# Optimization experiments

Hardware: AMD Instinct MI355X
Metric: run time of the kernel (lower is better)

The kernel has to match this reference:

```python
import jax, jax.numpy as jnp
import numpy as np

FEATS = 1024
HEAD = 16
MLP_HIDDEN = 4096
HEAD_DIM = FEATS // HEAD
SQRT_D = float(FEATS) ** 0.5  # module scales by sqrt(feats), not sqrt(head_dim)
LN_EPS = 1e-5


def layer_norm(x, g, b):
    mu = jnp.mean(x, axis=-1, keepdims=True)
    var = jnp.mean(jnp.square(x - mu), axis=-1, keepdims=True)
    return (x - mu) * jax.lax.rsqrt(var + LN_EPS) * g + b


def setup_inputs() -> dict:
    key = jax.random.key(0)
    ks = jax.random.split(key, 12)
    s = 1.0 / np.sqrt(FEATS)
    s2 = 1.0 / np.sqrt(MLP_HIDDEN)
    return {
        "x": jax.random.normal(ks[0], (2, 2048, FEATS), dtype=jnp.float32),
        "ln1_g": jnp.ones((FEATS,), jnp.float32),
        "ln1_b": jnp.zeros((FEATS,), jnp.float32),
        "wq": jax.random.normal(ks[1], (FEATS, FEATS), jnp.float32) * s,
        "bq": jnp.zeros((FEATS,), jnp.float32),
        "wk": jax.random.normal(ks[2], (FEATS, FEATS), jnp.float32) * s,
        "bk": jnp.zeros((FEATS,), jnp.float32),
        "wv": jax.random.normal(ks[3], (FEATS, FEATS), jnp.float32) * s,
        "bv": jnp.zeros((FEATS,), jnp.float32),
        "wo": jax.random.normal(ks[4], (FEATS, FEATS), jnp.float32) * s,
        "bo": jnp.zeros((FEATS,), jnp.float32),
        "ln2_g": jnp.ones((FEATS,), jnp.float32),
        "ln2_b": jnp.zeros((FEATS,), jnp.float32),
        "w1": jax.random.normal(ks[5], (MLP_HIDDEN, FEATS), jnp.float32) * s,
        "b1": jnp.zeros((MLP_HIDDEN,), jnp.float32),
        "w2": jax.random.normal(ks[6], (FEATS, MLP_HIDDEN), jnp.float32) * s2,
        "b2": jnp.zeros((FEATS,), jnp.float32),
    }


def reference(x, ln1_g, ln1_b, wq, bq, wk, bk, wv, bv, wo, bo,
              ln2_g, ln2_b, w1, b1, w2, b2):
    b, n, f = x.shape
    h = layer_norm(x, ln1_g, ln1_b)
    # qkv projections (torch Linear: y = x @ W.T + b)
    q = (h @ wq.T + bq).reshape(b, n, HEAD, HEAD_DIM).transpose(0, 2, 1, 3)
    k = (h @ wk.T + bk).reshape(b, n, HEAD, HEAD_DIM).transpose(0, 2, 1, 3)
    v = (h @ wv.T + bv).reshape(b, n, HEAD, HEAD_DIM).transpose(0, 2, 1, 3)
    score = jax.nn.softmax(jnp.einsum('bhif,bhjf->bhij', q, k) / SQRT_D, axis=-1)
    attn = jnp.einsum('bhij,bhjf->bihf', score, v).reshape(b, n, f)
    o = attn @ wo.T + bo
    out1 = o + x
    h2 = layer_norm(out1, ln2_g, ln2_b)
    mlp = jax.nn.relu(jax.nn.relu(h2 @ w1.T + b1) @ w2.T + b2)
    return mlp + out1
```

## Files before the change

### kernel.cpp

```cpp
#include <hip/hip_runtime.h>
#include <hip/hip_bf16.h>

#define FEATS 1024
#define NH 16
#define HD 64
#define SEQ 2048
#define BATCH 2
#define MTOT (BATCH*SEQ)
#define MLPH 4096
#define QSCALE 0.04508422277369218f

typedef __attribute__((ext_vector_type(8))) short bf16x8;
typedef __attribute__((ext_vector_type(4))) float f32x4;

static_assert(sizeof(bf16x8) == 16, "bf16x8 must be 16B");

__device__ __forceinline__ unsigned short f2bf(float f) {
    unsigned int u = __float_as_uint(f);
    unsigned int lsb = (u >> 16) & 1u;
    u += 0x7fffu + lsb;
    return (unsigned short)(u >> 16);
}
__device__ __forceinline__ float bf2f(unsigned short u) {
    return __uint_as_float((unsigned)u << 16);
}

#define ASYNC16(GP, LP) __builtin_amdgcn_global_load_lds( \
    (const __attribute__((address_space(1))) void*)(GP),  \
    (__attribute__((address_space(3))) void*)(LP), 16, 0, 0)

#define WAIT_VM(N) asm volatile("s_waitcnt vmcnt(" #N ")" ::: "memory")

__global__ __launch_bounds__(256) void cvt_all_kernel(
    const float* __restrict__ wq, const float* __restrict__ wk,
    const float* __restrict__ wv, const float* __restrict__ wo,
    const float* __restrict__ w1, const float* __restrict__ w2,
    unsigned short* __restrict__ dst) {
    const size_t i = ((size_t)blockIdx.x * 256 + threadIdx.x) * 4;
    const size_t MB = (size_t)1024 * 1024;
    const float* s;
    size_t off;
    float sc = 1.0f;
    if (i < MB)            { s = wq; off = i;          sc = QSCALE; }
    else if (i < 2 * MB)   { s = wk; off = i - MB; }
    else if (i < 3 * MB)   { s = wv; off = i - 2 * MB; }
    else if (i < 4 * MB)   { s = wo; off = i - 3 * MB; }
    else if (i < 8 * MB)   { s = w1; off = i - 4 * MB; }
    else                   { s = w2; off = i - 8 * MB; }
    float4 v = *(const float4*)(s + off);
    ushort4 o;
    o.x = f2bf(v.x * sc); o.y = f2bf(v.y * sc);
    o.z = f2bf(v.z * sc); o.w = f2bf(v.w * sc);
    *(ushort4*)(dst + i) = o;
}

__global__ __launch_bounds__(256) void concat3_kernel(const float* __restrict__ a,
                                                      const float* __restrict__ b,
                                                      const float* __restrict__ c,
                                                      float* __restrict__ o) {
    int i = blockIdx.x * 256 + threadIdx.x;
    float v = (i < 1024) ? a[i] * QSCALE : ((i < 2048) ? b[i - 1024] : c[i - 2048]);
    o[i] = v;
}

template <bool INBF16>
__global__ __launch_bounds__(256) void ln_kernel(const void* __restrict__ xin,
                                                 const float* __restrict__ g,
                                                 const float* __restrict__ bta,
                                                 unsigned short* __restrict__ h) {
    __shared__ float red[8];
    const int row = blockIdx.x;
    const int t = threadIdx.x;
    float4 v;
    if (INBF16) {
        const unsigned short* xr = (const unsigned short*)xin + (size_t)row * FEATS;
        ushort4 u = ((const ushort4*)xr)[t];
        v.x = bf2f(u.x); v.y = bf2f(u.y); v.z = bf2f(u.z); v.w = bf2f(u.w);
    } else {
        const float* xr = (const float*)xin + (size_t)row * FEATS;
        v = ((const float4*)xr)[t];
    }
    float s  = v.x + v.y + v.z + v.w;
    float ss = v.x * v.x + v.y * v.y + v.z * v.z + v.w * v.w;
#pragma unroll
    for (int off = 1; off < 64; off <<= 1) {
        s  += __shfl_xor(s, off);
        ss += __shfl_xor(ss, off);
    }
    const int w = t >> 6;
    if ((t & 63) == 0) { red[w] = s; red[4 + w] = ss; }
    __syncthreads();
    s  = red[0] + red[1] + red[2] + red[3];
    ss = red[4] + red[5] + red[6] + red[7];
    const float mu  = s * (1.f / FEATS);
    const float var = ss * (1.f / FEATS) - mu * mu;
    const float rs  = rsqrtf(var + 1e-5f);
    float4 gv = ((const float4*)g)[t];
    float4 bv = ((const float4*)bta)[t];
    ushort4 ov;
    ov.x = f2bf((v.x - mu) * rs * gv.x + bv.x);
    ov.y = f2bf((v.y - mu) * rs * gv.y + bv.y);
    ov.z = f2bf((v.z - mu) * rs * gv.z + bv.z);
    ov.w = f2bf((v.w - mu) * rs * gv.w + bv.w);
    ((ushort4*)h)[(size_t)row * (FEATS / 4) + t] = ov;
}

template <int DEPTH, bool RELU, bool ADDF32, bool ADDBF16, bool OUTBF16, bool VTRANS>
__global__ __launch_bounds__(256, (DEPTH == 2 ? 4 : DEPTH == 3 ? 3 : 2))
void gemm_kernel(const unsigned short* __restrict__ A,
                 const unsigned short* __restrict__ W,
                 const float* __restrict__ bias,
                 const void* __restrict__ addend,
                 void* __restrict__ outp,
                 unsigned short* __restrict__ vtp,
                 int M, int N, int K, int gx) {
    __shared__ unsigned short lds[DEPTH][2][128 * 32];

    const int t = threadIdx.x;
    const int w = t >> 6, lane = t & 63;
    const int wr = w >> 1, wc = w & 1;
    const int li = lane & 15, lj = lane >> 4;

    const int nwg = gridDim.x;
    const int cpx = nwg >> 3;
    const int wg = blockIdx.x;
    const int swz = (wg & 7) * cpx + (wg >> 3);
    const int mb = (swz / gx) * 128, nb = (swz % gx) * 128;

    const int srow = lane >> 2;
    const int scg = ((lane & 3) ^ (srow & 3)) * 8;
    const unsigned short* gA = A + (size_t)(mb + w * 16 + srow) * K + scg;
    const unsigned short* gB = W + (size_t)(nb + w * 16 + srow) * K + scg;
    const size_t half = (size_t)64 * K;
    const int lbase = w * 512 + lane * 8;

    const int rsw = (lj ^ (li & 3)) * 8;

    const int nt = K >> 5;

#define STAGE(BUF, K0)                                             \
    do {                                                           \
        unsigned short* la_ = &lds[BUF][0][lbase];                 \
        unsigned short* lb_ = &lds[BUF][1][lbase];                 \
        ASYNC16(gA + (K0), la_);                                   \
        ASYNC16(gA + half + (K0), la_ + 2048);                     \
        ASYNC16(gB + (K0), lb_);                                   \
        ASYNC16(gB + half + (K0), lb_ + 2048);                     \
    } while (0)

#pragma unroll
    for (int j = 0; j < DEPTH - 1; ++j)
        STAGE(j, j * 32);
    if constexpr (DEPTH == 2)      WAIT_VM(0);
    else if constexpr (DEPTH == 3) WAIT_VM(4);
    else                           WAIT_VM(8);
    __builtin_amdgcn_s_barrier();

    f32x4 acc[4][4] = {};

    for (int i = 0; i < nt; ++i) {
        const int cur = i % DEPTH;
        const unsigned short* Al = &lds[cur][0][0];
        const unsigned short* Bl = &lds[cur][1][0];

        bf16x8 af[4], bfr[4];
#pragma unroll
        for (int m = 0; m < 4; m++)
            af[m] = *(const bf16x8*)(Al + (wr * 64 + m * 16 + li) * 32 + rsw);
#pragma unroll
        for (int n = 0; n < 4; n++)
            bfr[n] = *(const bf16x8*)(Bl + (wc * 64 + n * 16 + li) * 32 + rsw);

        const int pft = i + DEPTH - 1;
        if (pft < nt) STAGE(pft % DEPTH, pft * 32);

#pragma unroll
        for (int m = 0; m < 4; m++)
#pragma unroll
            for (int n = 0; n < 4; n++)
                acc[m][n] = __builtin_amdgcn_mfma_f32_16x16x32_bf16(af[m], bfr[n], acc[m][n], 0, 0, 0);

        if (i + 1 < nt) {
            const int avail = (nt - 2) - i;
            const int rem = avail < (DEPTH - 2) ? avail : (DEPTH - 2);
            if (rem >= DEPTH - 2) {
                if constexpr (DEPTH == 2)      WAIT_VM(0);
                else if constexpr (DEPTH == 3) WAIT_VM(4);
                else                           WAIT_VM(8);
            }
            else if (rem == 1) WAIT_VM(4);
            else               WAIT_VM(0);
            __builtin_amdgcn_s_barrier();
        }
    }
#undef STAGE

#pragma unroll
    for (int m = 0; m < 4; m++) {
#pragma unroll
        for (int n = 0; n < 4; n++) {
            const int col = nb + wc * 64 + n * 16 + li;
            const float bv = bias[col];
            if (VTRANS && col >= 2048) {
                const int d2 = col - 2048;
                const int h2 = d2 >> 6, dd = d2 & 63;
                const int rowb = mb + wr * 64 + m * 16 + lj * 4;
                const int bb = rowb >> 11;
                const int s0 = rowb & (SEQ - 1);
                const int pos = (s0 & ~31) | (((s0 >> 2) & 3) << 3) | (((s0 >> 4) & 1) << 2);
                ushort4 vv;
                vv.x = f2bf(acc[m][n][0] + bv);
                vv.y = f2bf(acc[m][n][1] + bv);
                vv.z = f2bf(acc[m][n][2] + bv);
                vv.w = f2bf(acc[m][n][3] + bv);
                *(ushort4*)(vtp + ((size_t)(bb * NH + h2) * HD + dd) * SEQ + pos) = vv;
                continue;
            }
#pragma unroll
            for (int r = 0; r < 4; r++) {
                const int row = mb + wr * 64 + m * 16 + lj * 4 + r;
                float v = acc[m][n][r] + bv;
                if (RELU) v = fmaxf(v, 0.f);
                if (ADDF32)
                    v += ((const float*)addend)[(size_t)row * N + col];
                if (ADDBF16)
                    v += bf2f(((const unsigned short*)addend)[(size_t)row * N + col]);
                if (OUTBF16)
                    ((unsigned short*)outp)[(size_t)row * N + col] = f2bf(v);
                else
                    ((float*)outp)[(size_t)row * N + col] = v;
            }
        }
    }
}

__global__ __launch_bounds__(256, 4)
void attn_kernel(const unsigned short* __restrict__ qkv,
                 const unsigned short* __restrict__ vt,
                 unsigned short* __restrict__ out) {
    constexpr int LK = 72;
    __shared__ unsigned short Kl[2][64 * LK];
    __shared__ unsigned short Vtl[2][64 * LK];

    const int bh = blockIdx.x;
    const int b = bh >> 4, h = bh & 15;
    const int q0 = blockIdx.y * 128;
    const int t = threadIdx.x, w = t >> 6, lane = t & 63;
    const int li = lane & 15, lj = lane >> 4;

    const size_t rstr = 3 * FEATS;
    const unsigned short* qkvb = qkv + (size_t)(b * SEQ) * rstr;
    const unsigned short* ksrc = qkvb + FEATS + h * HD;
    const unsigned short* vsrc = vt + (size_t)bh * HD * SEQ;

    bf16x8 aq[2][2];
#pragma unroll
    for (int hh = 0; hh < 2; hh++)
#pragma unroll
        for (int kk = 0; kk < 2; kk++)
            aq[hh][kk] = *(const bf16x8*)(qkvb +
                (size_t)(q0 + w * 32 + hh * 16 + li) * rstr + h * HD + kk * 32 + lj * 8);

    f32x4 o[2][4] = {};
    f32x4 oS[2] = {};

    const short onebf = (short)0x3F80;
    const bf16x8 ones = {onebf, onebf, onebf, onebf, onebf, onebf, onebf, onebf};

    const int sr = t >> 2, sc = (t & 3) * 16;
    const unsigned short* kg = ksrc + (size_t)sr * rstr + sc;
    const unsigned short* vg = vsrc + (size_t)sr * SEQ + sc;
    const int ldo = sr * LK + sc;

    const int nt = SEQ / 64;

    {
        bf16x8 k0 = *(const bf16x8*)kg;
        bf16x8 k1 = *(const bf16x8*)(kg + 8);
        bf16x8 v0 = *(const bf16x8*)vg;
        bf16x8 v1 = *(const bf16x8*)(vg + 8);
        *(bf16x8*)(&Kl[0][ldo])      = k0;
        *(bf16x8*)(&Kl[0][ldo + 8])  = k1;
        *(bf16x8*)(&Vtl[0][ldo])     = v0;
        *(bf16x8*)(&Vtl[0][ldo + 8]) = v1;
    }

    int cur = 0;
    for (int i = 0; i < nt; ++i) {
        bf16x8 kr0, kr1, vr0, vr1;
        if (i + 1 < nt) {
            const unsigned short* kn = kg + (size_t)(i + 1) * 64 * rstr;
            const unsigned short* vn = vg + (i + 1) * 64;
            kr0 = *(const bf16x8*)kn;
            kr1 = *(const bf16x8*)(kn + 8);
            vr0 = *(const bf16x8*)vn;
            vr1 = *(const bf16x8*)(vn + 8);
        }

        asm volatile("s_waitcnt lgkmcnt(0)" ::: "memory");
        __builtin_amdgcn_s_barrier();

        const unsigned short* Kc = Kl[cur];
        const unsigned short* Vc = Vtl[cur];

        f32x4 s[2][4];
        __builtin_amdgcn_s_setprio(1);
#pragma unroll
        for (int n = 0; n < 4; n++) {
            bf16x8 k0 = *(const bf16x8*)(Kc + (n * 16 + li) * LK + lj * 8);
            bf16x8 k1 = *(const bf16x8*)(Kc + (n * 16 + li) * LK + 32 + lj * 8);
#pragma unroll
            for (int hh = 0; hh < 2; hh++) {
                f32x4 acc = {};
                acc = __builtin_amdgcn_mfma_f32_16x16x32_bf16(k0, aq[hh][0], acc, 0, 0, 0);
                acc = __builtin_amdgcn_mfma_f32_16x16x32_bf16(k1, aq[hh][1], acc, 0, 0, 0);
                s[hh][n] = acc;
            }
        }
        __builtin_amdgcn_s_setprio(0);

        bf16x8 A[2][2];
#pragma unroll
        for (int hh = 0; hh < 2; hh++)
#pragma unroll
            for (int kk = 0; kk < 2; kk++) {
                float p[8];
#pragma unroll
                for (int r = 0; r < 4; r++) {
                    p[r]     = exp2f(s[hh][2 * kk][r]);
                    p[4 + r] = exp2f(s[hh][2 * kk + 1][r]);
                }
                union { unsigned u[4]; bf16x8 v; } Au;
                asm("v_cvt_pk_bf16_f32 %0, %1, %2" : "=v"(Au.u[0]) : "v"(p[0]), "v"(p[1]));
                asm("v_cvt_pk_bf16_f32 %0, %1, %2" : "=v"(Au.u[1]) : "v"(p[2]), "v"(p[3]));
                asm("v_cvt_pk_bf16_f32 %0, %1, %2" : "=v"(Au.u[2]) : "v"(p[4]), "v"(p[5]));
                asm("v_cvt_pk_bf16_f32 %0, %1, %2" : "=v"(Au.u[3]) : "v"(p[6]), "v"(p[7]));
                A[hh][kk] = Au.v;
            }

#pragma unroll
        for (int hh = 0; hh < 2; hh++)
#pragma unroll
            for (int kk = 0; kk < 2; kk++)
                oS[hh] = __builtin_amdgcn_mfma_f32_16x16x32_bf16(A[hh][kk], ones, oS[hh], 0, 0, 0);

        __builtin_amdgcn_s_setprio(1);
#pragma unroll
        for (int n = 0; n < 4; n++) {
#pragma unroll
            for (int kk = 0; kk < 2; kk++) {
                bf16x8 bv = *(const bf16x8*)(Vc + (n * 16 + li) * LK + kk * 32 + lj * 8);
                o[0][n] = __builtin_amdgcn_mfma_f32_16x16x32_bf16(A[0][kk], bv, o[0][n], 0, 0, 0);
                o[1][n] = __builtin_amdgcn_mfma_f32_16x16x32_bf16(A[1][kk], bv, o[1][n], 0, 0, 0);
            }
        }
        __builtin_amdgcn_s_setprio(0);

        if (i + 1 < nt) {
            *(bf16x8*)(&Kl[cur ^ 1][ldo])      = kr0;
            *(bf16x8*)(&Kl[cur ^ 1][ldo + 8])  = kr1;
            *(bf16x8*)(&Vtl[cur ^ 1][ldo])     = vr0;
            *(bf16x8*)(&Vtl[cur ^ 1][ldo + 8]) = vr1;
        }
        cur ^= 1;
    }

    unsigned short* ob = out + (size_t)(b * SEQ + q0 + w * 32) * FEATS + h * HD;
#pragma unroll
    for (int hh = 0; hh < 2; hh++)
#pragma unroll
        for (int r = 0; r < 4; r++) {
            const float inv = 1.f / oS[hh][r];
#pragma unroll
            for (int n = 0; n < 4; n++)
                ob[(size_t)(hh * 16 + lj * 4 + r) * FEATS + n * 16 + li] =
                    f2bf(o[hh][n][r] * inv);
        }
}

extern "C" void kernel_launch(void* const* d_in, const int* in_sizes, int n_in,
                              void* d_out, int out_size, void* d_ws, size_t ws_size,
                              hipStream_t stream) {
    const float* x     = (const float*)d_in[0];
    const float* ln1_g = (const float*)d_in[1];
    const float* ln1_b = (const float*)d_in[2];
    const float* wq    = (const float*)d_in[3];
    const float* bq    = (const float*)d_in[4];
    const float* wk    = (const float*)d_in[5];
    const float* bk    = (const float*)d_in[6];
    const float* wv    = (const float*)d_in[7];
    const float* bvv   = (const float*)d_in[8];
    const float* wo    = (const float*)d_in[9];
    const float* bo    = (const float*)d_in[10];
    const float* ln2_g = (const float*)d_in[11];
    const float* ln2_b = (const float*)d_in[12];
    const float* w1    = (const float*)d_in[13];
    const float* b1    = (const float*)d_in[14];
    const float* w2    = (const float*)d_in[15];
    const float* b2    = (const float*)d_in[16];

    constexpr size_t MBs = 512 * 1024;
    unsigned short* ws16   = (unsigned short*)d_ws;
    unsigned short* wqkv_b = ws16;
    unsigned short* wo_b   = ws16 + 6 * MBs;
    unsigned short* w1_b   = ws16 + 8 * MBs;
    unsigned short* w2_b   = ws16 + 16 * MBs;
    unsigned short* qkvb   = ws16 + 24 * MBs;
    unsigned short* hb     = ws16 + 48 * MBs;
    unsigned short* a1     = ws16 + 24 * MBs;
    unsigned short* attn_o = ws16 + 56 * MBs;
    unsigned short* h2     = attn_o;
    unsigned short* out1b  = ws16 + 64 * MBs;
    unsigned short* vtb    = ws16 + 72 * MBs;
    float*          bqkv   = (float*)(ws16 + 80 * MBs);
    float*          outf   = (float*)d_out;

    dim3 blk(256);

    cvt_all_kernel<<<12288, blk, 0, stream>>>(wq, wk, wv, wo, w1, w2, wqkv_b);
    concat3_kernel<<<12, blk, 0, stream>>>(bq, bk, bvv, bqkv);

    ln_kernel<false><<<MTOT, blk, 0, stream>>>(x, ln1_g, ln1_b, hb);

    gemm_kernel<3, false, false, false, true, true><<<768, blk, 0, stream>>>(
        hb, wqkv_b, bqkv, nullptr, qkvb, vtb, MTOT, 3072, FEATS, 24);

    attn_kernel<<<dim3(BATCH * NH, SEQ / 128), blk, 0, stream>>>(qkvb, vtb, attn_o);

    gemm_kernel<4, false, true, false, true, false><<<256, blk, 0, stream>>>(
        attn_o, wo_b, bo, x, out1b, nullptr, MTOT, FEATS, FEATS, 8);

    ln_kernel<true><<<MTOT, blk, 0, stream>>>(out1b, ln2_g, ln2_b, h2);

    gemm_kernel<2, true, false, false, true, false><<<1024, blk, 0, stream>>>(
        h2, w1_b, b1, nullptr, a1, nullptr, MTOT, MLPH, FEATS, 32);

    gemm_kernel<4, true, false, true, false, false><<<256, blk, 0, stream>>>(
        a1, w2_b, b2, out1b, outf, nullptr, MTOT, FEATS, MLPH, 8);
}
```

Before: 226.7 us.

## Use async global-to-LDS loads with XOR swizzle in attention K/V staging

Result: no change. 223.9 us (median of 3 runs) (-1.2%).

```diff
diff --git a/kernel.cpp b/kernel.cpp
--- a/kernel.cpp
+++ b/kernel.cpp
@@ -238,15 +238,15 @@
 void attn_kernel(const unsigned short* __restrict__ qkv,
                  const unsigned short* __restrict__ vt,
                  unsigned short* __restrict__ out) {
-    constexpr int LK = 72;
-    __shared__ unsigned short Kl[2][64 * LK];
-    __shared__ unsigned short Vtl[2][64 * LK];
+    __shared__ unsigned short Kl[2][64 * 64];
+    __shared__ unsigned short Vtl[2][64 * 64];
 
     const int bh = blockIdx.x;
     const int b = bh >> 4, h = bh & 15;
     const int q0 = blockIdx.y * 128;
     const int t = threadIdx.x, w = t >> 6, lane = t & 63;
     const int li = lane & 15, lj = lane >> 4;
+    const int e7 = li & 7;
 
     const size_t rstr = 3 * FEATS;
     const unsigned short* qkvb = qkv + (size_t)(b * SEQ) * rstr;
@@ -267,38 +267,29 @@
     const short onebf = (short)0x3F80;
     const bf16x8 ones = {onebf, onebf, onebf, onebf, onebf, onebf, onebf, onebf};
 
-    const int sr = t >> 2, sc = (t & 3) * 16;
-    const unsigned short* kg = ksrc + (size_t)sr * rstr + sc;
-    const unsigned short* vg = vsrc + (size_t)sr * SEQ + sc;
-    const int ldo = sr * LK + sc;
+    const int srow = t >> 3;
+    const int sslot = (t & 7) ^ (srow & 7);
+    const unsigned short* kg = ksrc + (size_t)srow * rstr + sslot * 8;
+    const unsigned short* vg = vsrc + (size_t)srow * SEQ + sslot * 8;
+    const int ldst = t * 8;
+
+#define STAGEA(BUF, KV0)                                              \
+    do {                                                              \
+        ASYNC16(kg + (size_t)(KV0) * rstr, &Kl[BUF][ldst]);           \
+        ASYNC16(kg + (size_t)((KV0) + 32) * rstr, &Kl[BUF][ldst + 2048]); \
+        ASYNC16(vg + (KV0), &Vtl[BUF][ldst]);                         \
+        ASYNC16(vg + 32 * SEQ + (KV0), &Vtl[BUF][ldst + 2048]);       \
+    } while (0)
 
     const int nt = SEQ / 64;
 
-    {
-        bf16x8 k0 = *(const bf16x8*)kg;
-        bf16x8 k1 = *(const bf16x8*)(kg + 8);
-        bf16x8 v0 = *(const bf16x8*)vg;
-        bf16x8 v1 = *(const bf16x8*)(vg + 8);
-        *(bf16x8*)(&Kl[0][ldo])      = k0;
-        *(bf16x8*)(&Kl[0][ldo + 8])  = k1;
-        *(bf16x8*)(&Vtl[0][ldo])     = v0;
-        *(bf16x8*)(&Vtl[0][ldo + 8]) = v1;
-    }
+    STAGEA(0, 0);
+    WAIT_VM(0);
+    __builtin_amdgcn_s_barrier();
 
     int cur = 0;
     for (int i = 0; i < nt; ++i) {
-        bf16x8 kr0, kr1, vr0, vr1;
-        if (i + 1 < nt) {
-            const unsigned short* kn = kg + (size_t)(i + 1) * 64 * rstr;
-            const unsigned short* vn = vg + (i + 1) * 64;
-            kr0 = *(const bf16x8*)kn;
-            kr1 = *(const bf16x8*)(kn + 8);
-            vr0 = *(const bf16x8*)vn;
-            vr1 = *(const bf16x8*)(vn + 8);
-        }
-
-        asm volatile("s_waitcnt lgkmcnt(0)" ::: "memory");
-        __builtin_amdgcn_s_barrier();
+        if (i + 1 < nt) STAGEA(cur ^ 1, (i + 1) * 64);
 
         const unsigned short* Kc = Kl[cur];
         const unsigned short* Vc = Vtl[cur];
@@ -307,8 +298,9 @@
         __builtin_amdgcn_s_setprio(1);
 #pragma unroll
         for (int n = 0; n < 4; n++) {
-            bf16x8 k0 = *(const bf16x8*)(Kc + (n * 16 + li) * LK + lj * 8);
-            bf16x8 k1 = *(const bf16x8*)(Kc + (n * 16 + li) * LK + 32 + lj * 8);
+            const int rb = (n * 16 + li) * 64;
+            bf16x8 k0 = *(const bf16x8*)(Kc + rb + ((lj ^ e7) * 8));
+            bf16x8 k1 = *(const bf16x8*)(Kc + rb + (((lj + 4) ^ e7) * 8));
 #pragma unroll
             for (int hh = 0; hh < 2; hh++) {
                 f32x4 acc = {};
@@ -347,23 +339,23 @@
         __builtin_amdgcn_s_setprio(1);
 #pragma unroll
         for (int n = 0; n < 4; n++) {
-#pragma unroll
-            for (int kk = 0; kk < 2; kk++) {
-                bf16x8 bv = *(const bf16x8*)(Vc + (n * 16 + li) * LK + kk * 32 + lj * 8);
-                o[0][n] = __builtin_amdgcn_mfma_f32_16x16x32_bf16(A[0][kk], bv, o[0][n], 0, 0, 0);
-                o[1][n] = __builtin_amdgcn_mfma_f32_16x16x32_bf16(A[1][kk], bv, o[1][n], 0, 0, 0);
-            }
+            const int rb = (n * 16 + li) * 64;
+            bf16x8 bv0 = *(const bf16x8*)(Vc + rb + ((lj ^ e7) * 8));
+            bf16x8 bv1 = *(const bf16x8*)(Vc + rb + (((lj + 4) ^ e7) * 8));
+            o[0][n] = __builtin_amdgcn_mfma_f32_16x16x32_bf16(A[0][0], bv0, o[0][n], 0, 0, 0);
+            o[1][n] = __builtin_amdgcn_mfma_f32_16x16x32_bf16(A[1][0], bv0, o[1][n], 0, 0, 0);
+            o[0][n] = __builtin_amdgcn_mfma_f32_16x16x32_bf16(A[0][1], bv1, o[0][n], 0, 0, 0);
+            o[1][n] = __builtin_amdgcn_mfma_f32_16x16x32_bf16(A[1][1], bv1, o[1][n], 0, 0, 0);
         }
         __builtin_amdgcn_s_setprio(0);
 
         if (i + 1 < nt) {
-            *(bf16x8*)(&Kl[cur ^ 1][ldo])      = kr0;
-            *(bf16x8*)(&Kl[cur ^ 1][ldo + 8])  = kr1;
-            *(bf16x8*)(&Vtl[cur ^ 1][ldo])     = vr0;
-            *(bf16x8*)(&Vtl[cur ^ 1][ldo + 8]) = vr1;
+            WAIT_VM(0);
+            __builtin_amdgcn_s_barrier();
         }
         cur ^= 1;
     }
+#undef STAGEA
 
     unsigned short* ob = out + (size_t)(b * SEQ + q0 + w * 32) * FEATS + h * HD;
 #pragma unroll
```
